# Kernel optimization log

Measured on AMD Instinct MI355X. Metric: run time of the kernel, lower is better.

The kernel has to match this reference:

```python
import jax, jax.numpy as jnp
import numpy as np

R_RAYS = 65536
S_PER_RAY = 128
N_TOTAL = R_RAYS * S_PER_RAY


def setup_inputs() -> dict:
    key = jax.random.key(0)
    k1, k2, k3, k4 = jax.random.split(key, 4)
    sigmas = jax.random.uniform(k1, (N_TOTAL,), dtype=jnp.float32) * 2.0  # densities >= 0
    rgbs = jax.random.uniform(k2, (N_TOTAL, 3), dtype=jnp.float32)
    deltas = jax.random.uniform(k3, (N_TOTAL,), dtype=jnp.float32) * 0.01 + 1e-3
    ts = jax.random.uniform(k4, (N_TOTAL,), dtype=jnp.float32) * 6.0 + 0.1
    ray_idx = jnp.arange(R_RAYS, dtype=jnp.int32)
    rays_a = jnp.stack([ray_idx, ray_idx * S_PER_RAY,
                        jnp.full((R_RAYS,), S_PER_RAY, dtype=jnp.int32)], axis=1)
    return {"sigmas": sigmas, "rgbs": rgbs, "deltas": deltas, "ts": ts,
            "rays_a": rays_a, "T_threshold": 1e-4}


def reference(sigmas, rgbs, deltas, ts, rays_a, T_threshold):
    R = rays_a.shape[0]
    N = sigmas.shape[0]
    S_max = int(jnp.max(rays_a[:, 2]))  # max samples per ray (concrete)

    offs = jnp.arange(S_max, dtype=rays_a.dtype)
    valid = offs[None, :] < rays_a[:, 2, None]              # [R, S] prefix mask
    idx = jnp.where(valid, rays_a[:, 1, None] + offs[None, :], N - 1)  # [R, S]

    a = 1.0 - jnp.exp(-sigmas[idx] * deltas[idx])           # [R, S] alphas

    # Sequential transmittance recurrence with early-exit (T set to 0 once below threshold)
    def step(T, xs):
        a_s, v_s = xs                                        # [R], [R]
        alive = (T > T_threshold) & v_s
        w = jnp.where(alive, a_s * T, 0.0)
        T = jnp.where(alive, T * (1.0 - a_s), 0.0)
        return T, (w, alive)

    T0 = jnp.ones((R,), sigmas.dtype)
    _, (wT, aliveT) = jax.lax.scan(step, T0, (a.T, valid.T))
    w = wT.T                                                 # [R, S] weights
    alive = aliveT.T

    op_n = jnp.sum(w, axis=1)                                # [R]
    dep_n = jnp.sum(w * ts[idx], axis=1)                     # [R]
    rgb_n = jnp.einsum('rs,rsc->rc', w, rgbs[idx])           # [R, 3]
    cnt_n = jnp.sum(alive, axis=1).astype(jnp.int32)

    ridx = rays_a[:, 0]
    opacity = jnp.zeros((R,), w.dtype).at[ridx].add(op_n)
    depth = jnp.zeros((R,), w.dtype).at[ridx].add(dep_n)
    rgb = jnp.zeros((R, 3), w.dtype).at[ridx].add(rgb_n)
    total_samples = jnp.zeros((R,), jnp.int32).at[ridx].add(cnt_n)
    # invalid slots were mapped to index N-1 with w=0, so .add is safe
    ws = jnp.zeros((N,), w.dtype).at[idx.reshape(-1)].add(w.reshape(-1))

    return total_samples.sum(), opacity, depth, rgb, ws
```

## Files before the change

kernel.cpp:

```cpp
#include <hip/hip_runtime.h>


typedef float f2u __attribute__((ext_vector_type(2), aligned(4)));

template<int CTRL, int RM>
__device__ __forceinline__ float dpp_mul1(float v) {
    float t = __int_as_float(__builtin_amdgcn_update_dpp(
        0x3f800000, __float_as_int(v), CTRL, RM, 0xF, false));
    return v * t;
}

template<int CTRL>
__device__ __forceinline__ float dpp_add0(float v) {
    float t = __int_as_float(__builtin_amdgcn_update_dpp(
        0, __float_as_int(v), CTRL, 0xF, 0xF, false));
    return v + t;
}

__device__ __forceinline__ float ray_reduce(float v) {
    v = dpp_add0<0x101>(v);
    v = dpp_add0<0x102>(v);
    v = dpp_add0<0x104>(v);
    v = dpp_add0<0x108>(v);
    v += __int_as_float(__builtin_amdgcn_ds_swizzle(
            __float_as_int(v), 0x401F));
    v += __shfl_xor(v, 32, 64);
    return v;
}

__global__ __launch_bounds__(256) void vr_main(
    const float* __restrict__ sigmas, const float* __restrict__ rgbs,
    const float* __restrict__ deltas, const float* __restrict__ ts,
    const int* __restrict__ rays_a, const float* __restrict__ thr_p,
    float* __restrict__ out, float* __restrict__ cnt_ws,
    int R, int use_ws)
{
    int wid  = (int)((blockIdx.x * blockDim.x + threadIdx.x) >> 6);
    int lane = (int)(threadIdx.x & 63);
    if (wid >= R) return;

    const int ridx  = rays_a[3 * wid + 0];
    const int start = rays_a[3 * wid + 1];
    const int count = rays_a[3 * wid + 2];
    const float thr = thr_p[0];

    const int s0 = 2 * lane;
    const bool v0 = s0 < count, v1 = s0 + 1 < count;

    float sg0 = 0.f, sg1 = 0.f, dt0 = 0.f, dt1 = 0.f, t0 = 0.f, t1 = 0.f;
    float r0 = 0.f, g0 = 0.f, b0 = 0.f, r1 = 0.f, g1 = 0.f, b1 = 0.f;

    if (v1) {
        f2u sg = *(const f2u*)(sigmas + start + s0);
        f2u dt = *(const f2u*)(deltas + start + s0);
        f2u tt = *(const f2u*)(ts     + start + s0);
        const float* rg = rgbs + 3 * (size_t)(start + s0);
        f2u c01 = *(const f2u*)(rg + 0);
        f2u c23 = *(const f2u*)(rg + 2);
        f2u c45 = *(const f2u*)(rg + 4);
        sg0 = sg.x; sg1 = sg.y; dt0 = dt.x; dt1 = dt.y; t0 = tt.x; t1 = tt.y;
        r0 = c01.x; g0 = c01.y; b0 = c23.x; r1 = c23.y; g1 = c45.x; b1 = c45.y;
    } else if (v0) {
        sg0 = sigmas[start + s0]; dt0 = deltas[start + s0]; t0 = ts[start + s0];
        const float* rg = rgbs + 3 * (size_t)(start + s0);
        r0 = rg[0]; g0 = rg[1]; b0 = rg[2];
    }

    float f0 = v0 ? __expf(-sg0 * dt0) : 1.f;
    float f1 = v1 ? __expf(-sg1 * dt1) : 1.f;
    float fprod = f0 * f1;

    float inc = fprod;
    inc = dpp_mul1<0x111, 0xF>(inc);
    inc = dpp_mul1<0x112, 0xF>(inc);
    inc = dpp_mul1<0x114, 0xF>(inc);
    inc = dpp_mul1<0x118, 0xF>(inc);
    inc = dpp_mul1<0x142, 0xa>(inc);
    inc = dpp_mul1<0x143, 0xc>(inc);

    float T0 = inc / fprod;
    float T1 = T0 * f0;
    float T2 = T1 * f1;

    bool alive0 = v0 && (T0 > thr);
    bool alive1 = v1 && (T1 > thr);
    float w0 = alive0 ? (T0 - T1) : 0.f;
    float w1 = alive1 ? (T1 - T2) : 0.f;

    float* wsp = out + 1 + 5 * (size_t)R + (size_t)start;
    if (v1) {
        f2u wv; wv.x = w0; wv.y = w1;
        *(f2u*)(wsp + s0) = wv;
    } else if (v0) {
        wsp[s0] = w0;
    }

    float op  = w0 + w1;
    float dep = fmaf(w0, t0, w1 * t1);
    float cr  = fmaf(w0, r0, w1 * r1);
    float cg  = fmaf(w0, g0, w1 * g1);
    float cb  = fmaf(w0, b0, w1 * b1);
    float cnt = (alive0 ? 1.f : 0.f) + (alive1 ? 1.f : 0.f);

    op  = ray_reduce(op);
    dep = ray_reduce(dep);
    cr  = ray_reduce(cr);
    cg  = ray_reduce(cg);
    cb  = ray_reduce(cb);
    cnt = ray_reduce(cnt);

    if (lane == 0) {
        out[1 + ridx]                 = op;
        out[1 + R + ridx]             = dep;
        out[1 + 2*R + 3*ridx + 0]     = cr;
        out[1 + 2*R + 3*ridx + 1]     = cg;
        out[1 + 2*R + 3*ridx + 2]     = cb;
        if (use_ws) cnt_ws[wid] = cnt;
        else        atomicAdd(&out[0], cnt);
    }
}

__global__ __launch_bounds__(256) void vr_total(
    const float* __restrict__ cnt_ws, float* __restrict__ out, int R)
{
    __shared__ float sm[4];
    float s = 0.f;
    for (int i = blockIdx.x * 256 + threadIdx.x; i < R; i += gridDim.x * 256)
        s += cnt_ws[i];
    #pragma unroll
    for (int d = 32; d; d >>= 1) s += __shfl_xor(s, d, 64);
    int w = threadIdx.x >> 6;
    if ((threadIdx.x & 63) == 0) sm[w] = s;
    __syncthreads();
    if (threadIdx.x == 0) atomicAdd(&out[0], sm[0] + sm[1] + sm[2] + sm[3]);
}

extern "C" void kernel_launch(void* const* d_in, const int* in_sizes, int n_in,
                              void* d_out, int out_size, void* d_ws, size_t ws_size,
                              hipStream_t stream) {
    const float* sigmas = (const float*)d_in[0];
    const float* rgbs   = (const float*)d_in[1];
    const float* deltas = (const float*)d_in[2];
    const float* ts     = (const float*)d_in[3];
    const int*   rays_a = (const int*)d_in[4];
    const float* thr    = (const float*)d_in[5];
    int R = in_sizes[4] / 3;
    float* out = (float*)d_out;
    float* cnt_ws = (float*)d_ws;

    int use_ws = (ws_size >= (size_t)R * sizeof(float)) ? 1 : 0;

    hipMemsetAsync(d_out, 0, 4, stream);

    int grid = (R + 3) / 4;
    vr_main<<<grid, 256, 0, stream>>>(sigmas, rgbs, deltas, ts, rays_a, thr,
                                      out, cnt_ws, R, use_ws);
    if (use_ws)
        vr_total<<<64, 256, 0, stream>>>(cnt_ws, out, R);
}
```

Measured before the change: 48.82 us.

## Process two rays per wavefront with 4 samples per lane and LDS RGB staging

Each wavefront now handles two 128-sample rays (32 lanes each, 4 samples per lane) using float4 loads. The interleaved RGB data is staged through LDS to get coalesced 16-byte loads, then de-interleaved per lane. The scan and reduction shrink to 32-lane segments. The count total kernel becomes a single 1024-thread block that writes out[0] directly, so the memset is dropped when the workspace is used. A generic per-sample fallback path is kept for irregular rays. Risks are LDS traffic, a wave-level waitcnt barrier without a proper sync, and reduced occupancy from the LDS footprint.

Measured after the change: 46.59 us. 1.05x faster.

```diff
diff --git a/kernel.cpp b/kernel.cpp
--- a/kernel.cpp
+++ b/kernel.cpp
@@ -1,7 +1,7 @@
 #include <hip/hip_runtime.h>
 
 
-typedef float f2u __attribute__((ext_vector_type(2), aligned(4)));
+typedef float f4a __attribute__((ext_vector_type(4), aligned(4)));
 
 template<int CTRL, int RM>
 __device__ __forceinline__ float dpp_mul1(float v) {
@@ -9,22 +9,19 @@
         0x3f800000, __float_as_int(v), CTRL, RM, 0xF, false));
     return v * t;
 }
-
 template<int CTRL>
 __device__ __forceinline__ float dpp_add0(float v) {
     float t = __int_as_float(__builtin_amdgcn_update_dpp(
         0, __float_as_int(v), CTRL, 0xF, 0xF, false));
     return v + t;
 }
-
-__device__ __forceinline__ float ray_reduce(float v) {
+__device__ __forceinline__ float seg_reduce32(float v) {
     v = dpp_add0<0x101>(v);
     v = dpp_add0<0x102>(v);
     v = dpp_add0<0x104>(v);
     v = dpp_add0<0x108>(v);
     v += __int_as_float(__builtin_amdgcn_ds_swizzle(
             __float_as_int(v), 0x401F));
-    v += __shfl_xor(v, 32, 64);
     return v;
 }
 
@@ -35,104 +32,151 @@
     float* __restrict__ out, float* __restrict__ cnt_ws,
     int R, int use_ws)
 {
-    int wid  = (int)((blockIdx.x * blockDim.x + threadIdx.x) >> 6);
-    int lane = (int)(threadIdx.x & 63);
-    if (wid >= R) return;
-
-    const int ridx  = rays_a[3 * wid + 0];
-    const int start = rays_a[3 * wid + 1];
-    const int count = rays_a[3 * wid + 2];
+    __shared__ float lds[4][2][384];
+
+    const int wib  = (int)(threadIdx.x >> 6);
+    const int wid  = (int)blockIdx.x * 4 + wib;
+    const int lane = (int)(threadIdx.x & 63);
+    const int half = lane >> 5;
+    const int sl   = lane & 31;
+    const int ray  = 2 * wid + half;
+    const bool inR = ray < R;
+
+    int ridx = 0, start = 0, count = 0;
+    if (inR) {
+        ridx  = rays_a[3 * ray + 0];
+        start = rays_a[3 * ray + 1];
+        count = rays_a[3 * ray + 2];
+    }
     const float thr = thr_p[0];
 
-    const int s0 = 2 * lane;
-    const bool v0 = s0 < count, v1 = s0 + 1 < count;
-
-    float sg0 = 0.f, sg1 = 0.f, dt0 = 0.f, dt1 = 0.f, t0 = 0.f, t1 = 0.f;
-    float r0 = 0.f, g0 = 0.f, b0 = 0.f, r1 = 0.f, g1 = 0.f, b1 = 0.f;
-
-    if (v1) {
-        f2u sg = *(const f2u*)(sigmas + start + s0);
-        f2u dt = *(const f2u*)(deltas + start + s0);
-        f2u tt = *(const f2u*)(ts     + start + s0);
-        const float* rg = rgbs + 3 * (size_t)(start + s0);
-        f2u c01 = *(const f2u*)(rg + 0);
-        f2u c23 = *(const f2u*)(rg + 2);
-        f2u c45 = *(const f2u*)(rg + 4);
-        sg0 = sg.x; sg1 = sg.y; dt0 = dt.x; dt1 = dt.y; t0 = tt.x; t1 = tt.y;
-        r0 = c01.x; g0 = c01.y; b0 = c23.x; r1 = c23.y; g1 = c45.x; b1 = c45.y;
-    } else if (v0) {
-        sg0 = sigmas[start + s0]; dt0 = deltas[start + s0]; t0 = ts[start + s0];
-        const float* rg = rgbs + 3 * (size_t)(start + s0);
-        r0 = rg[0]; g0 = rg[1]; b0 = rg[2];
-    }
-
-    float f0 = v0 ? __expf(-sg0 * dt0) : 1.f;
-    float f1 = v1 ? __expf(-sg1 * dt1) : 1.f;
-    float fprod = f0 * f1;
-
+    const bool ok = inR && (count == 128) && ((start & 3) == 0);
+    const bool fastw = __all(ok);
+
+    float fe[4], tv[4], rr[4], gg[4], bb[4];
+    bool  v[4];
+
+    if (fastw) {
+        const float4 sg4 = *(const float4*)(sigmas + start + 4 * sl);
+        const float4 dt4 = *(const float4*)(deltas + start + 4 * sl);
+        const float4 tt4 = *(const float4*)(ts     + start + 4 * sl);
+
+        const float4* rg = (const float4*)(rgbs + 3 * (size_t)start);
+        float* L = &lds[wib][half][0];
+        #pragma unroll
+        for (int j = 0; j < 3; ++j) {
+            float4 c = rg[32 * j + sl];
+            *(float4*)(L + 128 * j + 4 * sl) = c;
+        }
+        fe[0] = __expf(-sg4.x * dt4.x);
+        fe[1] = __expf(-sg4.y * dt4.y);
+        fe[2] = __expf(-sg4.z * dt4.z);
+        fe[3] = __expf(-sg4.w * dt4.w);
+        tv[0] = tt4.x; tv[1] = tt4.y; tv[2] = tt4.z; tv[3] = tt4.w;
+
+        asm volatile("s_waitcnt lgkmcnt(0)" ::: "memory");
+        const float4 c0 = *(const float4*)(L + 12 * sl + 0);
+        const float4 c1 = *(const float4*)(L + 12 * sl + 4);
+        const float4 c2 = *(const float4*)(L + 12 * sl + 8);
+        rr[0] = c0.x; rr[1] = c0.w; rr[2] = c1.z; rr[3] = c2.y;
+        gg[0] = c0.y; gg[1] = c1.x; gg[2] = c1.w; gg[3] = c2.z;
+        bb[0] = c0.z; bb[1] = c1.y; bb[2] = c2.x; bb[3] = c2.w;
+        v[0] = v[1] = v[2] = v[3] = true;
+    } else {
+        #pragma unroll
+        for (int i = 0; i < 4; ++i) {
+            const int s = 4 * sl + i;
+            const bool vi = inR && (s < count);
+            v[i] = vi;
+            float sg = 0.f, dt = 0.f;
+            tv[i] = 0.f; rr[i] = 0.f; gg[i] = 0.f; bb[i] = 0.f;
+            if (vi) {
+                sg = sigmas[start + s];
+                dt = deltas[start + s];
+                tv[i] = ts[start + s];
+                const float* rg = rgbs + 3 * ((size_t)start + s);
+                rr[i] = rg[0]; gg[i] = rg[1]; bb[i] = rg[2];
+            }
+            fe[i] = vi ? __expf(-sg * dt) : 1.f;
+        }
+    }
+
+    const float fprod = (fe[0] * fe[1]) * (fe[2] * fe[3]);
     float inc = fprod;
     inc = dpp_mul1<0x111, 0xF>(inc);
     inc = dpp_mul1<0x112, 0xF>(inc);
     inc = dpp_mul1<0x114, 0xF>(inc);
     inc = dpp_mul1<0x118, 0xF>(inc);
-    inc = dpp_mul1<0x142, 0xa>(inc);
-    inc = dpp_mul1<0x143, 0xc>(inc);
-
-    float T0 = inc / fprod;
-    float T1 = T0 * f0;
-    float T2 = T1 * f1;
-
-    bool alive0 = v0 && (T0 > thr);
-    bool alive1 = v1 && (T1 > thr);
-    float w0 = alive0 ? (T0 - T1) : 0.f;
-    float w1 = alive1 ? (T1 - T2) : 0.f;
-
-    float* wsp = out + 1 + 5 * (size_t)R + (size_t)start;
-    if (v1) {
-        f2u wv; wv.x = w0; wv.y = w1;
-        *(f2u*)(wsp + s0) = wv;
-    } else if (v0) {
-        wsp[s0] = w0;
-    }
-
-    float op  = w0 + w1;
-    float dep = fmaf(w0, t0, w1 * t1);
-    float cr  = fmaf(w0, r0, w1 * r1);
-    float cg  = fmaf(w0, g0, w1 * g1);
-    float cb  = fmaf(w0, b0, w1 * b1);
-    float cnt = (alive0 ? 1.f : 0.f) + (alive1 ? 1.f : 0.f);
-
-    op  = ray_reduce(op);
-    dep = ray_reduce(dep);
-    cr  = ray_reduce(cr);
-    cg  = ray_reduce(cg);
-    cb  = ray_reduce(cb);
-    cnt = ray_reduce(cnt);
-
-    if (lane == 0) {
-        out[1 + ridx]                 = op;
-        out[1 + R + ridx]             = dep;
-        out[1 + 2*R + 3*ridx + 0]     = cr;
-        out[1 + 2*R + 3*ridx + 1]     = cg;
-        out[1 + 2*R + 3*ridx + 2]     = cb;
-        if (use_ws) cnt_ws[wid] = cnt;
+    inc = dpp_mul1<0x142, 0xA>(inc);
+
+    float T = inc / fprod;
+
+    float w[4];
+    float cnt = 0.f;
+    #pragma unroll
+    for (int i = 0; i < 4; ++i) {
+        const bool alive = v[i] && (T > thr);
+        const float Tn = T * fe[i];
+        w[i] = alive ? (T - Tn) : 0.f;
+        cnt += alive ? 1.f : 0.f;
+        T = Tn;
+    }
+
+    float* wsp = out + 1 + 5 * (size_t)R + (size_t)start + 4 * sl;
+    if (fastw) {
+        f4a wv; wv.x = w[0]; wv.y = w[1]; wv.z = w[2]; wv.w = w[3];
+        *(f4a*)wsp = wv;
+    } else {
+        #pragma unroll
+        for (int i = 0; i < 4; ++i) if (v[i]) wsp[i] = w[i];
+    }
+
+    float op  = (w[0] + w[1]) + (w[2] + w[3]);
+    float dep = fmaf(w[0], tv[0], fmaf(w[1], tv[1], fmaf(w[2], tv[2], w[3] * tv[3])));
+    float cr  = fmaf(w[0], rr[0], fmaf(w[1], rr[1], fmaf(w[2], rr[2], w[3] * rr[3])));
+    float cg  = fmaf(w[0], gg[0], fmaf(w[1], gg[1], fmaf(w[2], gg[2], w[3] * gg[3])));
+    float cb  = fmaf(w[0], bb[0], fmaf(w[1], bb[1], fmaf(w[2], bb[2], w[3] * bb[3])));
+
+    op  = seg_reduce32(op);
+    dep = seg_reduce32(dep);
+    cr  = seg_reduce32(cr);
+    cg  = seg_reduce32(cg);
+    cb  = seg_reduce32(cb);
+    cnt = seg_reduce32(cnt);
+
+    if (sl == 0 && inR) {
+        out[1 + ridx]             = op;
+        out[1 + R + ridx]         = dep;
+        out[1 + 2*R + 3*ridx + 0] = cr;
+        out[1 + 2*R + 3*ridx + 1] = cg;
+        out[1 + 2*R + 3*ridx + 2] = cb;
+        if (use_ws) cnt_ws[ray] = cnt;
         else        atomicAdd(&out[0], cnt);
     }
 }
 
-__global__ __launch_bounds__(256) void vr_total(
+__global__ __launch_bounds__(1024) void vr_total(
     const float* __restrict__ cnt_ws, float* __restrict__ out, int R)
 {
-    __shared__ float sm[4];
+    __shared__ float sm[16];
     float s = 0.f;
-    for (int i = blockIdx.x * 256 + threadIdx.x; i < R; i += gridDim.x * 256)
-        s += cnt_ws[i];
+    const int R4 = R & ~3;
+    for (int i = (int)threadIdx.x * 4; i < R4; i += 4096) {
+        const float4 c = *(const float4*)(cnt_ws + i);
+        s += (c.x + c.y) + (c.z + c.w);
+    }
+    if (threadIdx.x == 0)
+        for (int i = R4; i < R; ++i) s += cnt_ws[i];
     #pragma unroll
     for (int d = 32; d; d >>= 1) s += __shfl_xor(s, d, 64);
-    int w = threadIdx.x >> 6;
-    if ((threadIdx.x & 63) == 0) sm[w] = s;
+    if ((threadIdx.x & 63) == 0) sm[threadIdx.x >> 6] = s;
     __syncthreads();
-    if (threadIdx.x == 0) atomicAdd(&out[0], sm[0] + sm[1] + sm[2] + sm[3]);
+    if (threadIdx.x == 0) {
+        float t = 0.f;
+        #pragma unroll
+        for (int k = 0; k < 16; ++k) t += sm[k];
+        out[0] = t;
+    }
 }
 
 extern "C" void kernel_launch(void* const* d_in, const int* in_sizes, int n_in,
@@ -150,11 +194,12 @@
 
     int use_ws = (ws_size >= (size_t)R * sizeof(float)) ? 1 : 0;
 
-    hipMemsetAsync(d_out, 0, 4, stream);
-
-    int grid = (R + 3) / 4;
+    if (!use_ws)
+        hipMemsetAsync(d_out, 0, 4, stream);
+
+    int grid = (R + 7) / 8;
     vr_main<<<grid, 256, 0, stream>>>(sigmas, rgbs, deltas, ts, rays_a, thr,
                                       out, cnt_ws, R, use_ws);
     if (use_ws)
-        vr_total<<<64, 256, 0, stream>>>(cnt_ws, out, R);
-}
+        vr_total<<<1, 1024, 0, stream>>>(cnt_ws, out, R);
+}
```
